# Optimization experiments

Measured on AMD Instinct MI355X. Metric: run time of the kernel, lower is better.

Reference implementation:

```python
import jax, jax.numpy as jnp
import numpy as np

# static config (matches init_kwargs)
B, HID, NH, D = 1, 1024, 16, 64
T, Hh, W = 8, 32, 32
TT, TH, TW = 2, 8, 8            # tile sizes (numel 128)
WT, WH, WW = 6 // TT, 16 // TH, 16 // TW  # window in tiles: 3,2,2
NTT, NTH, NTW = T // TT, Hh // TH, W // TW  # 4,4,4
NTILE = NTT * NTH * NTW          # 64
TILE = TT * TH * TW              # 128
WK = WT * WH * WW                # 12 kv tiles per q tile
S = T * Hh * W


def _dim_window(nt, w):
    left = w // 2
    right = w // 2 + (w % 2) - 1
    center = jnp.clip(jnp.arange(nt), left, nt - 1 - right)
    return center[:, None] - left + jnp.arange(w)  # [nt, w]


def _kv_tile_idx():
    kt = _dim_window(NTT, WT)  # [NTT, WT]
    kh = _dim_window(NTH, WH)  # [NTH, WH]
    kw = _dim_window(NTW, WW)  # [NTW, WW]
    idx = (kt[:, None, None, :, None, None] * (NTH * NTW)
           + kh[None, :, None, None, :, None] * NTW
           + kw[None, None, :, None, None, :])
    return idx.reshape(NTILE, WK)


def _to_tiles(x, nh):
    # [B, S, nh*D] -> [B, nh, NTILE, TILE, D]; seq laid out (ntt tt nth th ntw tw)
    x = x.reshape(B, NTT, TT, NTH, TH, NTW, TW, nh, D)
    x = x.transpose(0, 7, 1, 3, 5, 2, 4, 6, 8)
    return x.reshape(B, nh, NTILE, TILE, D)


def _from_tiles(o):
    # [B, NH, NTILE, TILE, D] -> [B, S, NH*D]
    o = o.reshape(B, NH, NTT, NTH, NTW, TT, TH, TW, D)
    o = o.transpose(0, 2, 5, 3, 6, 4, 7, 1, 8)
    return o.reshape(B, S, NH * D)


def setup_inputs() -> dict:
    key = jax.random.key(0)
    ks = jax.random.split(key, 5)
    sc = 1.0 / np.sqrt(HID)
    return {
        'hidden_states': jax.random.normal(ks[0], (B, S, HID), jnp.float32),
        'wq': jax.random.normal(ks[1], (HID, NH * D), jnp.float32) * sc,
        'wk': jax.random.normal(ks[2], (HID, NH * D), jnp.float32) * sc,
        'wv': jax.random.normal(ks[3], (HID, NH * D), jnp.float32) * sc,
        'wo': jax.random.normal(ks[4], (NH * D, HID), jnp.float32) * sc,
    }


def reference(hidden_states, wq, wk, wv, wo):
    kv_idx = _kv_tile_idx()  # [NTILE, WK]
    q = _to_tiles(hidden_states @ wq, NH)  # [B,NH,NTILE,TILE,D]
    k = _to_tiles(hidden_states @ wk, NH)
    v = _to_tiles(hidden_states @ wv, NH)
    # gather each query tile's exact kv window (mask fully satisfied by construction)
    kg = k[:, :, kv_idx].reshape(B, NH, NTILE, WK * TILE, D)
    vg = v[:, :, kv_idx].reshape(B, NH, NTILE, WK * TILE, D)
    scores = jnp.einsum('bhnqd,bhnkd->bhnqk', q, kg) * (1.0 / np.sqrt(D))
    p = jax.nn.softmax(scores, axis=-1)
    o = jnp.einsum('bhnqk,bhnkd->bhnqd', p, vg)
    return _from_tiles(o) @ wo
```

## Files before the change

kernel.cpp:

```cpp
#include <hip/hip_runtime.h>
#include <hip/hip_bf16.h>
#include <math.h>

typedef __attribute__((ext_vector_type(8))) short          short8;
typedef __attribute__((ext_vector_type(8))) unsigned short u16x8;
typedef __attribute__((ext_vector_type(2))) unsigned int   u32x2;
typedef __attribute__((ext_vector_type(4))) float          f32x4;

#define MFMA_BF16(a, b, c) __builtin_amdgcn_mfma_f32_16x16x32_bf16((a), (b), (c), 0, 0, 0)

#define GLOAD_LDS16(gp, lp)                                        \
  __builtin_amdgcn_global_load_lds(                                \
      (const __attribute__((address_space(1))) void*)(gp),         \
      (__attribute__((address_space(3))) void*)(lp), 16, 0, 0)


__device__ __forceinline__ unsigned short f2bf(float f) {
  union { float f; unsigned int u; } v; v.f = f;
  unsigned int r = v.u + 0x7fffu + ((v.u >> 16) & 1u);
  return (unsigned short)(r >> 16);
}
__device__ __forceinline__ unsigned int pack2bf(float a, float b) {
  union { float f; unsigned int u; } x, y; x.f = a; y.f = b;
  return ((x.u + 0x8000u) >> 16) | ((y.u + 0x8000u) & 0xffff0000u);
}

__device__ __forceinline__ int row_to_seq(int r) {
  int tile = r >> 7, pos = r & 127;
  int ntt = tile >> 4, nth = (tile >> 2) & 3, ntw = tile & 3;
  int tt  = pos >> 6,  th  = (pos >> 3) & 7,  tw  = pos & 7;
  return ((ntt * 2 + tt) << 10) | ((nth * 8 + th) << 5) | (ntw * 8 + tw);
}

__global__ __launch_bounds__(256) void permute_hs(const float* __restrict__ in,
                                                  unsigned short* __restrict__ out) {
  int cid = blockIdx.x * 256 + threadIdx.x;
  int r = cid >> 7, c = (cid & 127) * 8;
  int s = row_to_seq(r);
  const float* f = in + (size_t)s * 1024 + c;
  u16x8 v;
#pragma unroll
  for (int j = 0; j < 8; ++j) v[j] = f2bf(f[j]);
  *(u16x8*)(out + (size_t)r * 1024 + c) = v;
}

__global__ __launch_bounds__(256) void transpose_w(const float* __restrict__ w0,
                                                   const float* __restrict__ w1,
                                                   const float* __restrict__ w2,
                                                   const float* __restrict__ w3,
                                                   unsigned short* __restrict__ out) {
  __shared__ unsigned short Lt[64 * 68];
  int m = blockIdx.y;
  const float* W = (m == 0) ? w0 : (m == 1) ? w1 : (m == 2) ? w2 : w3;
  unsigned short* O = out + (size_t)m * 1048576;
  int k0 = (blockIdx.x >> 4) * 64, n0 = (blockIdx.x & 15) * 64;
  int tid = threadIdx.x;
#pragma unroll
  for (int i = 0; i < 2; ++i) {
    int cid = i * 256 + tid;
    int kr = cid >> 3, c = cid & 7;
    const float* f = W + (size_t)(k0 + kr) * 1024 + n0 + c * 8;
#pragma unroll
    for (int j = 0; j < 8; ++j) Lt[(c * 8 + j) * 68 + kr] = f2bf(f[j]);
  }
  __syncthreads();
#pragma unroll
  for (int i = 0; i < 2; ++i) {
    int cid = i * 256 + tid;
    int nr = cid >> 3, c = cid & 7;
    u16x8 v;
#pragma unroll
    for (int j = 0; j < 8; ++j) v[j] = Lt[nr * 68 + c * 8 + j];
    *(u16x8*)(O + (size_t)(n0 + nr) * 1024 + k0 + c * 8) = v;
  }
}

template <int SCATTER, int OUT_F32>
__device__ __forceinline__ void gemm_bt_body(const unsigned short* __restrict__ A,
                                             const unsigned short* __restrict__ Bt,
                                             void* __restrict__ Cv,
                                             int row0, int col0, float scale) {
  __shared__ unsigned short As[128 * 64];
  __shared__ unsigned short Bs[128 * 64];
  const int tid  = threadIdx.x;
  const int lane = tid & 63, w = tid >> 6;
  const int quad = lane >> 4, lm = lane & 15;
  const int wr = (w >> 1) * 64, wc = (w & 1) * 64;
  f32x4 acc[4][4] = {};
  for (int kt = 0; kt < 16; ++kt) {
    const int k0 = kt * 64;
    __syncthreads();
#pragma unroll
    for (int i = 0; i < 4; ++i) {
      int cid = i * 256 + tid;
      int r = cid >> 3, c = cid & 7;
      int cg = c ^ (r & 7);
      int base = (i * 256 + (tid & 192)) * 8;
      GLOAD_LDS16(A  + (size_t)(row0 + r) * 1024 + k0 + cg * 8, As + base);
      GLOAD_LDS16(Bt + (size_t)(col0 + r) * 1024 + k0 + cg * 8, Bs + base);
    }
    __syncthreads();
#pragma unroll
    for (int kh = 0; kh < 2; ++kh) {
      short8 af[4], bf[4];
#pragma unroll
      for (int t = 0; t < 4; ++t) {
        int ca = (kh * 4 + quad) ^ (lm & 7);
        af[t] = *(const short8*)(As + (wr + t * 16 + lm) * 64 + ca * 8);
        bf[t] = *(const short8*)(Bs + (wc + t * 16 + lm) * 64 + ca * 8);
      }
#pragma unroll
      for (int rt = 0; rt < 4; ++rt)
#pragma unroll
        for (int ct = 0; ct < 4; ++ct)
          acc[rt][ct] = MFMA_BF16(af[rt], bf[ct], acc[rt][ct]);
    }
  }
#pragma unroll
  for (int rt = 0; rt < 4; ++rt)
#pragma unroll
    for (int ct = 0; ct < 4; ++ct)
#pragma unroll
      for (int g = 0; g < 4; ++g) {
        int R  = row0 + wr + rt * 16 + quad * 4 + g;
        int Cc = col0 + wc + ct * 16 + lm;
        int Rs = SCATTER ? row_to_seq(R) : R;
        float vv = acc[rt][ct][g] * scale;
        if (OUT_F32) ((float*)Cv)[(size_t)Rs * 1024 + Cc] = vv;
        else ((unsigned short*)Cv)[(size_t)Rs * 1024 + Cc] = f2bf(vv);
      }
}

__global__ __launch_bounds__(256) void gemm_qkv(const unsigned short* __restrict__ A,
                                                const unsigned short* __restrict__ Wt,
                                                unsigned short* __restrict__ QKV) {
  float scale = (blockIdx.z == 0) ? 0.18033688011112042f : 1.0f;
  gemm_bt_body<0, 0>(A, Wt + (size_t)blockIdx.z * 1048576,
                     QKV + (size_t)blockIdx.z * 8388608,
                     blockIdx.y * 128, blockIdx.x * 128, scale);
}

__global__ __launch_bounds__(256) void gemm_out(const unsigned short* __restrict__ A,
                                                const unsigned short* __restrict__ Wt,
                                                float* __restrict__ Cout) {
  gemm_bt_body<1, 1>(A, Wt, Cout, blockIdx.y * 128, blockIdx.x * 128, 1.0f);
}

__global__ __launch_bounds__(256) void transpose_v(const unsigned short* __restrict__ V,
                                                   unsigned short* __restrict__ Vt) {
  __shared__ unsigned short Lt[64 * 136];
  int kt = blockIdx.x, h = blockIdx.y, tid = threadIdx.x;
#pragma unroll
  for (int i = 0; i < 4; ++i) {
    int cid = i * 256 + tid;
    int r = cid >> 3, c = cid & 7;
    u16x8 v = *(const u16x8*)(V + (size_t)(kt * 128 + r) * 1024 + h * 64 + c * 8);
#pragma unroll
    for (int j = 0; j < 8; ++j) Lt[(c * 8 + j) * 136 + r] = v[j];
  }
  __syncthreads();
#pragma unroll
  for (int i = 0; i < 4; ++i) {
    int cid = i * 256 + tid;
    int d = cid >> 4, c = cid & 15;
    u16x8 v = *(const u16x8*)(Lt + d * 136 + c * 8);
    *(u16x8*)(Vt + (size_t)(h * 64 + d) * 8192 + kt * 128 + c * 8) = v;
  }
}

__global__ __launch_bounds__(256) void attn(const unsigned short* __restrict__ Q,
                                            const unsigned short* __restrict__ K,
                                            const unsigned short* __restrict__ Vt,
                                            unsigned short* __restrict__ O) {
  __shared__ unsigned short Vs[64 * 128];
  __shared__ unsigned short KsPb[4 * 32 * 136];

  const int tid  = threadIdx.x;
  const int lane = tid & 63, w = tid >> 6;
  const int quad = lane >> 4, lm = lane & 15;
  unsigned short* Ks  = KsPb;
  unsigned short* Pbw = KsPb + w * (32 * 136);

  const int h = blockIdx.x >> 6, qt = blockIdx.x & 63;
  const int ntt = qt >> 4, nth = (qt >> 2) & 3, ntw = qt & 3;
  const int kt0 = min(max(ntt, 1), 2) - 1;
  const int kh0 = min(max(nth, 1), 3) - 1;
  const int kw0 = min(max(ntw, 1), 3) - 1;

  short8 bq[2][2];
#pragma unroll
  for (int ct = 0; ct < 2; ++ct)
#pragma unroll
    for (int kh = 0; kh < 2; ++kh)
      bq[ct][kh] = *(const short8*)(Q + (size_t)(qt * 128 + w * 32 + ct * 16 + lm) * 1024
                                      + h * 64 + kh * 32 + quad * 8);

  short8 ones8;
#pragma unroll
  for (int j = 0; j < 8; ++j) ones8[j] = (short)0x3F80;

  f32x4 o_acc[2][4] = {};
  f32x4 l_acc[2] = {};

  for (int it = 0; it < 12; ++it) {
    const int tt2 = it >> 2, hh2 = (it >> 1) & 1, ww2 = it & 1;
    const int kvt = (kt0 + tt2) * 16 + (kh0 + hh2) * 4 + (kw0 + ww2);
    __syncthreads();
#pragma unroll
    for (int i = 0; i < 4; ++i) {
      int cid = i * 256 + tid;
      int r = cid >> 3, c = cid & 7, cg = c ^ (r & 7);
      int base = (i * 256 + (tid & 192)) * 8;
      GLOAD_LDS16(K + (size_t)(kvt * 128 + r) * 1024 + h * 64 + cg * 8, Ks + base);
    }
#pragma unroll
    for (int i = 0; i < 4; ++i) {
      int cid = i * 256 + tid;
      int d = cid >> 4, c = cid & 15, cg = c ^ (d & 7);
      int base = (i * 256 + (tid & 192)) * 8;
      GLOAD_LDS16(Vt + (size_t)(h * 64 + d) * 8192 + kvt * 128 + cg * 8, Vs + base);
    }
    __syncthreads();

    f32x4 sa[2][8] = {};
#pragma unroll
    for (int kh = 0; kh < 2; ++kh) {
      short8 ak[8];
#pragma unroll
      for (int rt = 0; rt < 8; ++rt)
        ak[rt] = *(const short8*)(Ks + (rt * 16 + lm) * 64 + (((kh * 4 + quad) ^ (lm & 7)) * 8));
#pragma unroll
      for (int rt = 0; rt < 8; ++rt) {
        sa[0][rt] = MFMA_BF16(ak[rt], bq[0][kh], sa[0][rt]);
        sa[1][rt] = MFMA_BF16(ak[rt], bq[1][kh], sa[1][rt]);
      }
    }

    __syncthreads();

#pragma unroll
    for (int ct = 0; ct < 2; ++ct) {
      unsigned short* prow = Pbw + (ct * 16 + lm) * 136 + quad * 4;
#pragma unroll
      for (int rt = 0; rt < 8; ++rt) {
        float p0 = exp2f(sa[ct][rt][0]);
        float p1 = exp2f(sa[ct][rt][1]);
        float p2 = exp2f(sa[ct][rt][2]);
        float p3 = exp2f(sa[ct][rt][3]);
        u32x2 pk; pk[0] = pack2bf(p0, p1); pk[1] = pack2bf(p2, p3);
        *(u32x2*)(prow + rt * 16) = pk;
      }
    }

#pragma unroll
    for (int ks = 0; ks < 4; ++ks) {
      short8 ap0 = *(const short8*)(Pbw + (0 * 16 + lm) * 136 + ks * 32 + quad * 8);
      short8 ap1 = *(const short8*)(Pbw + (1 * 16 + lm) * 136 + ks * 32 + quad * 8);
      l_acc[0] = MFMA_BF16(ap0, ones8, l_acc[0]);
      l_acc[1] = MFMA_BF16(ap1, ones8, l_acc[1]);
#pragma unroll
      for (int nt = 0; nt < 4; ++nt) {
        short8 bv = *(const short8*)(Vs + (nt * 16 + lm) * 128 + (((ks * 4 + quad) ^ (lm & 7)) * 8));
        o_acc[0][nt] = MFMA_BF16(ap0, bv, o_acc[0][nt]);
        o_acc[1][nt] = MFMA_BF16(ap1, bv, o_acc[1][nt]);
      }
    }
  }

#pragma unroll
  for (int rt2 = 0; rt2 < 2; ++rt2)
#pragma unroll
    for (int g = 0; g < 4; ++g) {
      float inv = 1.0f / l_acc[rt2][g];
#pragma unroll
      for (int nt = 0; nt < 4; ++nt) {
        int R = qt * 128 + w * 32 + rt2 * 16 + quad * 4 + g;
        O[(size_t)R * 1024 + h * 64 + nt * 16 + lm] = f2bf(o_acc[rt2][nt][g] * inv);
      }
    }
}

extern "C" void kernel_launch(void* const* d_in, const int* in_sizes, int n_in,
                              void* d_out, int out_size, void* d_ws, size_t ws_size,
                              hipStream_t stream) {
  const float* hs = (const float*)d_in[0];
  const float* wq = (const float*)d_in[1];
  const float* wk = (const float*)d_in[2];
  const float* wv = (const float*)d_in[3];
  const float* wo = (const float*)d_in[4];
  float* out = (float*)d_out;

  const size_t NEL = 8388608;
  unsigned short* ws  = (unsigned short*)d_ws;
  unsigned short* HSt = ws;
  unsigned short* Qb  = ws + 1 * NEL;
  unsigned short* Kb  = ws + 2 * NEL;
  unsigned short* Vb  = ws + 3 * NEL;
  unsigned short* Vtb = ws + 4 * NEL;
  unsigned short* Ot  = ws + 5 * NEL;
  unsigned short* Wt  = ws + 6 * NEL;
  if (ws_size < (6 * NEL + 4 * 1048576) * sizeof(unsigned short)) return;

  permute_hs<<<4096, 256, 0, stream>>>(hs, HSt);
  transpose_w<<<dim3(256, 4), 256, 0, stream>>>(wq, wk, wv, wo, Wt);
  gemm_qkv<<<dim3(8, 64, 3), 256, 0, stream>>>(HSt, Wt, Qb);
  transpose_v<<<dim3(64, 16), 256, 0, stream>>>(Vb, Vtb);
  attn<<<1024, 256, 0, stream>>>(Qb, Kb, Vtb, Ot);
  gemm_out<<<dim3(8, 64, 1), 256, 0, stream>>>(Ot, Wt + 3 * 1048576, out);
  (void)in_sizes; (void)n_in; (void)out_size;
}
```

Measured before the change: 301.3 us.

## Use 8 waves of 16 query rows each in attention kernel

The attention block grows from 4 to 8 wavefronts, each handling 16 query rows instead of 32, which halves per-thread accumulator and score registers and raises the number of waves available to hide latency. The P staging buffer drops its padded stride in favour of an XOR swizzle to avoid LDS bank conflicts, and the K/V tile loads are split across twice as many threads. In exchange, each K and V fragment read from LDS feeds only one MFMA instead of two, so LDS read traffic per MFMA doubles.

```diff
diff --git a/kernel.cpp b/kernel.cpp
--- a/kernel.cpp
+++ b/kernel.cpp
@@ -168,18 +168,18 @@
   }
 }
 
-__global__ __launch_bounds__(256) void attn(const unsigned short* __restrict__ Q,
-                                            const unsigned short* __restrict__ K,
-                                            const unsigned short* __restrict__ Vt,
-                                            unsigned short* __restrict__ O) {
+__global__ __launch_bounds__(512, 4) void attn(const unsigned short* __restrict__ Q,
+                                               const unsigned short* __restrict__ K,
+                                               const unsigned short* __restrict__ Vt,
+                                               unsigned short* __restrict__ O) {
   __shared__ unsigned short Vs[64 * 128];
-  __shared__ unsigned short KsPb[4 * 32 * 136];
+  __shared__ unsigned short KsPb[8 * 16 * 128];
 
   const int tid  = threadIdx.x;
   const int lane = tid & 63, w = tid >> 6;
   const int quad = lane >> 4, lm = lane & 15;
   unsigned short* Ks  = KsPb;
-  unsigned short* Pbw = KsPb + w * (32 * 136);
+  unsigned short* Pbw = KsPb + w * 2048;
 
   const int h = blockIdx.x >> 6, qt = blockIdx.x & 63;
   const int ntt = qt >> 4, nth = (qt >> 2) & 3, ntw = qt & 3;
@@ -187,42 +187,40 @@
   const int kh0 = min(max(nth, 1), 3) - 1;
   const int kw0 = min(max(ntw, 1), 3) - 1;
 
-  short8 bq[2][2];
-#pragma unroll
-  for (int ct = 0; ct < 2; ++ct)
-#pragma unroll
-    for (int kh = 0; kh < 2; ++kh)
-      bq[ct][kh] = *(const short8*)(Q + (size_t)(qt * 128 + w * 32 + ct * 16 + lm) * 1024
-                                      + h * 64 + kh * 32 + quad * 8);
+  short8 bq[2];
+#pragma unroll
+  for (int kh = 0; kh < 2; ++kh)
+    bq[kh] = *(const short8*)(Q + (size_t)(qt * 128 + w * 16 + lm) * 1024
+                                + h * 64 + kh * 32 + quad * 8);
 
   short8 ones8;
 #pragma unroll
   for (int j = 0; j < 8; ++j) ones8[j] = (short)0x3F80;
 
-  f32x4 o_acc[2][4] = {};
-  f32x4 l_acc[2] = {};
+  f32x4 o_acc[4] = {};
+  f32x4 l_acc = {};
 
   for (int it = 0; it < 12; ++it) {
     const int tt2 = it >> 2, hh2 = (it >> 1) & 1, ww2 = it & 1;
     const int kvt = (kt0 + tt2) * 16 + (kh0 + hh2) * 4 + (kw0 + ww2);
     __syncthreads();
 #pragma unroll
-    for (int i = 0; i < 4; ++i) {
-      int cid = i * 256 + tid;
+    for (int i = 0; i < 2; ++i) {
+      int cid = i * 512 + tid;
       int r = cid >> 3, c = cid & 7, cg = c ^ (r & 7);
-      int base = (i * 256 + (tid & 192)) * 8;
+      int base = (i * 512 + (tid & 448)) * 8;
       GLOAD_LDS16(K + (size_t)(kvt * 128 + r) * 1024 + h * 64 + cg * 8, Ks + base);
     }
 #pragma unroll
-    for (int i = 0; i < 4; ++i) {
-      int cid = i * 256 + tid;
+    for (int i = 0; i < 2; ++i) {
+      int cid = i * 512 + tid;
       int d = cid >> 4, c = cid & 15, cg = c ^ (d & 7);
-      int base = (i * 256 + (tid & 192)) * 8;
+      int base = (i * 512 + (tid & 448)) * 8;
       GLOAD_LDS16(Vt + (size_t)(h * 64 + d) * 8192 + kvt * 128 + cg * 8, Vs + base);
     }
     __syncthreads();
 
-    f32x4 sa[2][8] = {};
+    f32x4 sa[8] = {};
 #pragma unroll
     for (int kh = 0; kh < 2; ++kh) {
       short8 ak[8];
@@ -230,54 +228,43 @@
       for (int rt = 0; rt < 8; ++rt)
         ak[rt] = *(const short8*)(Ks + (rt * 16 + lm) * 64 + (((kh * 4 + quad) ^ (lm & 7)) * 8));
 #pragma unroll
-      for (int rt = 0; rt < 8; ++rt) {
-        sa[0][rt] = MFMA_BF16(ak[rt], bq[0][kh], sa[0][rt]);
-        sa[1][rt] = MFMA_BF16(ak[rt], bq[1][kh], sa[1][rt]);
-      }
-    }
-
-    __syncthreads();
-
-#pragma unroll
-    for (int ct = 0; ct < 2; ++ct) {
-      unsigned short* prow = Pbw + (ct * 16 + lm) * 136 + quad * 4;
-#pragma unroll
-      for (int rt = 0; rt < 8; ++rt) {
-        float p0 = exp2f(sa[ct][rt][0]);
-        float p1 = exp2f(sa[ct][rt][1]);
-        float p2 = exp2f(sa[ct][rt][2]);
-        float p3 = exp2f(sa[ct][rt][3]);
-        u32x2 pk; pk[0] = pack2bf(p0, p1); pk[1] = pack2bf(p2, p3);
-        *(u32x2*)(prow + rt * 16) = pk;
-      }
+      for (int rt = 0; rt < 8; ++rt)
+        sa[rt] = MFMA_BF16(ak[rt], bq[kh], sa[rt]);
+    }
+
+    __syncthreads();
+
+#pragma unroll
+    for (int rt = 0; rt < 8; ++rt) {
+      float p0 = exp2f(sa[rt][0]);
+      float p1 = exp2f(sa[rt][1]);
+      float p2 = exp2f(sa[rt][2]);
+      float p3 = exp2f(sa[rt][3]);
+      u32x2 pk; pk[0] = pack2bf(p0, p1); pk[1] = pack2bf(p2, p3);
+      *(u32x2*)(Pbw + lm * 128 + (((2 * rt + (quad >> 1)) ^ (lm & 7)) * 8) + (quad & 1) * 4) = pk;
     }
 
 #pragma unroll
     for (int ks = 0; ks < 4; ++ks) {
-      short8 ap0 = *(const short8*)(Pbw + (0 * 16 + lm) * 136 + ks * 32 + quad * 8);
-      short8 ap1 = *(const short8*)(Pbw + (1 * 16 + lm) * 136 + ks * 32 + quad * 8);
-      l_acc[0] = MFMA_BF16(ap0, ones8, l_acc[0]);
-      l_acc[1] = MFMA_BF16(ap1, ones8, l_acc[1]);
+      short8 ap = *(const short8*)(Pbw + lm * 128 + (((4 * ks + quad) ^ (lm & 7)) * 8));
+      l_acc = MFMA_BF16(ap, ones8, l_acc);
 #pragma unroll
       for (int nt = 0; nt < 4; ++nt) {
         short8 bv = *(const short8*)(Vs + (nt * 16 + lm) * 128 + (((ks * 4 + quad) ^ (lm & 7)) * 8));
-        o_acc[0][nt] = MFMA_BF16(ap0, bv, o_acc[0][nt]);
-        o_acc[1][nt] = MFMA_BF16(ap1, bv, o_acc[1][nt]);
+        o_acc[nt] = MFMA_BF16(ap, bv, o_acc[nt]);
       }
     }
   }
 
 #pragma unroll
-  for (int rt2 = 0; rt2 < 2; ++rt2)
-#pragma unroll
-    for (int g = 0; g < 4; ++g) {
-      float inv = 1.0f / l_acc[rt2][g];
-#pragma unroll
-      for (int nt = 0; nt < 4; ++nt) {
-        int R = qt * 128 + w * 32 + rt2 * 16 + quad * 4 + g;
-        O[(size_t)R * 1024 + h * 64 + nt * 16 + lm] = f2bf(o_acc[rt2][nt][g] * inv);
-      }
-    }
+  for (int g = 0; g < 4; ++g) {
+    float inv = 1.0f / l_acc[g];
+#pragma unroll
+    for (int nt = 0; nt < 4; ++nt) {
+      int R = qt * 128 + w * 16 + quad * 4 + g;
+      O[(size_t)R * 1024 + h * 64 + nt * 16 + lm] = f2bf(o_acc[nt][g] * inv);
+    }
+  }
 }
 
 extern "C" void kernel_launch(void* const* d_in, const int* in_sizes, int n_in,
@@ -305,7 +292,7 @@
   transpose_w<<<dim3(256, 4), 256, 0, stream>>>(wq, wk, wv, wo, Wt);
   gemm_qkv<<<dim3(8, 64, 3), 256, 0, stream>>>(HSt, Wt, Qb);
   transpose_v<<<dim3(64, 16), 256, 0, stream>>>(Vb, Vtb);
-  attn<<<1024, 256, 0, stream>>>(Qb, Kb, Vtb, Ot);
+  attn<<<1024, 512, 0, stream>>>(Qb, Kb, Vtb, Ot);
   gemm_out<<<dim3(8, 64, 1), 256, 0, stream>>>(Ot, Wt + 3 * 1048576, out);
   (void)in_sizes; (void)n_in; (void)out_size;
 }
```

After: 300.3 us. No clear change (-0.3%).
